# Performance work log

Hardware: AMD Instinct MI355X
Metric: run time of the kernel (lower is better)

## Reference

```python
import jax, jax.numpy as jnp
import numpy as np
from jax import lax

K = 3          # kernel_size
G = 8          # group count in SIFA
EPS = 1e-5     # BN and GN eps


def _bn(x, g, b, m, v):
    # eval-mode BatchNorm2d over channel dim 1
    scale = (g / jnp.sqrt(v + EPS))[None, :, None, None]
    shift = (b - m * g / jnp.sqrt(v + EPS))[None, :, None, None]
    return x * scale + shift


def setup_inputs() -> dict:
    key = jax.random.key(0)
    ks = jax.random.split(key, 20)
    B, C, H, W, OUP = 8, 64, 128, 128, 128
    CE = C * K * K  # expanded channels = 576
    CG = C // G     # channels per group view = 8
    f32 = jnp.float32
    inp = {
        "x": jax.random.normal(ks[0], (B, C, H, W), f32),
        # depthwise generate conv: groups=C, out=C*K^2 -> OIHW [CE,1,K,K]
        "gen_w": jax.random.normal(ks[1], (CE, 1, K, K), f32) * 0.1,
        "gen_bn_g": jnp.ones((CE,), f32) + 0.1 * jax.random.normal(ks[2], (CE,), f32),
        "gen_bn_b": 0.1 * jax.random.normal(ks[3], (CE,), f32),
        "gen_bn_m": 0.05 * jax.random.normal(ks[4], (CE,), f32),
        "gen_bn_v": jax.random.uniform(ks[5], (CE,), f32, 0.5, 1.5),
        # GroupNorm(num_groups=CG, num_channels=CG) affine params
        "gn_w": jnp.ones((CG,), f32) + 0.1 * jax.random.normal(ks[6], (CG,), f32),
        "gn_b": 0.1 * jax.random.normal(ks[7], (CG,), f32),
        # gating params, shape (1, CG, 1, 1)
        "cweight": 0.1 * jax.random.normal(ks[8], (1, CG, 1, 1), f32),
        "cbias": jnp.ones((1, CG, 1, 1), f32) + 0.1 * jax.random.normal(ks[9], (1, CG, 1, 1), f32),
        "sweight": 0.1 * jax.random.normal(ks[10], (1, CG, 1, 1), f32),
        "sbias": jnp.ones((1, CG, 1, 1), f32) + 0.1 * jax.random.normal(ks[11], (1, CG, 1, 1), f32),
        "weights_add": jnp.asarray(0.5, f32),
        # final Conv: C -> OUP, k=K, s=K, p=0, bias=False + BN + SiLU
        "conv_w": jax.random.normal(ks[12], (OUP, C, K, K), f32) * (1.0 / np.sqrt(C * K * K)),
        "conv_bn_g": jnp.ones((OUP,), f32) + 0.1 * jax.random.normal(ks[13], (OUP,), f32),
        "conv_bn_b": 0.1 * jax.random.normal(ks[14], (OUP,), f32),
        "conv_bn_m": 0.05 * jax.random.normal(ks[15], (OUP,), f32),
        "conv_bn_v": jax.random.uniform(ks[16], (OUP,), f32, 0.5, 1.5),
    }
    return inp


def reference(x, gen_w, gen_bn_g, gen_bn_b, gen_bn_m, gen_bn_v,
              gn_w, gn_b, cweight, cbias, sweight, sbias, weights_add,
              conv_w, conv_bn_g, conv_bn_b, conv_bn_m, conv_bn_v):
    B, C, H, W = x.shape
    # --- generate: depthwise conv (groups=C) + BN + ReLU ---
    y = lax.conv_general_dilated(
        x, gen_w, window_strides=(1, 1), padding=[(K // 2, K // 2)] * 2,
        feature_group_count=C,
        dimension_numbers=("NCHW", "OIHW", "NCHW"))  # [B, C*K*K, H, W]
    y = jax.nn.relu(_bn(y, gen_bn_g, gen_bn_b, gen_bn_m, gen_bn_v))
    # --- rearrange 'b c (n1 n2) h w -> b c (h n1) (w n2)' ---
    y = y.reshape(B, C, K, K, H, W)          # (b, c, n1, n2, h, w)
    y = y.transpose(0, 1, 4, 2, 5, 3)        # (b, c, h, n1, w, n2)
    HK, WK = H * K, W * K
    y = y.reshape(B, C, HK, WK)
    # --- group view: (b*G, C//G, HK, WK) ---
    g = y.reshape(B * G, C // G, HK, WK)
    # channel gate: global avg pool -> affine -> sigmoid
    x_ch = jnp.mean(g, axis=(2, 3), keepdims=True)        # [B*G, CG, 1, 1]
    ch = g * jax.nn.sigmoid(cweight * x_ch + cbias)
    # spatial gate: per-channel GroupNorm (num_groups == num_channels)
    mu = jnp.mean(g, axis=(2, 3), keepdims=True)
    var = jnp.var(g, axis=(2, 3), keepdims=True)
    gnorm = (g - mu) / jnp.sqrt(var + EPS)
    gnorm = gnorm * gn_w[None, :, None, None] + gn_b[None, :, None, None]
    sp = g * jax.nn.sigmoid(sweight * gnorm + sbias)
    out = weights_add * ch + (1.0 - weights_add) * sp
    out = out.reshape(B, C, HK, WK)
    # --- final Conv: k=K, s=K, p=0, no bias + BN + SiLU ---
    z = lax.conv_general_dilated(
        out, conv_w, window_strides=(K, K), padding="VALID",
        dimension_numbers=("NCHW", "OIHW", "NCHW"))       # [B, OUP, H, W]
    z = _bn(z, conv_bn_g, conv_bn_b, conv_bn_m, conv_bn_v)
    return z * jax.nn.sigmoid(z)  # SiLU
```

## Files before the change

kernel.cpp:

```cpp
#include <hip/hip_runtime.h>
#include <math.h>


#define EPSF 1e-5f
typedef _Float16 v8h __attribute__((ext_vector_type(8)));
typedef __fp16 fp16x2 __attribute__((ext_vector_type(2)));
typedef float v4f __attribute__((ext_vector_type(4)));

static constexpr int C_ = 64, HW_ = 16384, W_ = 128;
static constexpr int KB_ = 80;

static constexpr int WS_WFOLD = 0;
static constexpr int WS_SHIFT = 5184;
static constexpr int WS_BIAS  = 5760;
static constexpr int WS_GATE  = 5888;
static constexpr int WS_PART  = 7936;
static constexpr int WS_WH    = 73472;
static constexpr int WS_BIMG  = 114688;
static constexpr size_t BIMG_BATCH_F16 = (size_t)128 * KB_ * 128 * 8;
static constexpr size_t BIMG_BATCH_FLT = BIMG_BATCH_F16 / 2;

__device__ __forceinline__ float sigmf(float v) { return 1.f / (1.f + __expf(-v)); }

__device__ __forceinline__ unsigned int pk_u32(float a, float b) {
    fp16x2 h = __builtin_amdgcn_cvt_pkrtz(a, b);
    return __builtin_bit_cast(unsigned int, h);
}

__global__ __launch_bounds__(256) void k_fold(
    const float* __restrict__ gen_w,
    const float* __restrict__ gg, const float* __restrict__ gb,
    const float* __restrict__ gm, const float* __restrict__ gv,
    const float* __restrict__ conv_w,
    const float* __restrict__ cg, const float* __restrict__ cb,
    const float* __restrict__ cm, const float* __restrict__ cv,
    float* __restrict__ ws)
{
    int idx = blockIdx.x * 256 + threadIdx.x;
    _Float16* Whp = (_Float16*)(ws + WS_WH);
    if (idx < 81920) {
        int kb = idx >> 10, oup = (idx >> 3) & 127, e = idx & 7;
        int k = kb * 8 + e;
        int grp = k / 80, rr = k - grp * 80;
        int tp = rr / 40, vv = rr - tp * 40;
        float v = 0.f;
        if (vv < 36) {
            int j = vv >> 2, cl = vv & 3, c = grp * 8 + tp * 4 + cl;
            float s = cg[oup] * rsqrtf(cv[oup] + EPSF);
            v = conv_w[(oup * C_ + c) * 9 + j] * s;
        }
        Whp[idx] = (_Float16)v;
    } else if (idx < 87104) {
        int i = idx - 81920; int ce = i / 9;
        float s = gg[ce] * rsqrtf(gv[ce] + EPSF);
        ws[WS_WFOLD + i] = gen_w[i] * s;
    } else if (idx < 87680) {
        int ce = idx - 87104;
        float s = gg[ce] * rsqrtf(gv[ce] + EPSF);
        ws[WS_SHIFT + ce] = gb[ce] - gm[ce] * s;
    } else if (idx < 87808) {
        int oup = idx - 87680;
        float s = cg[oup] * rsqrtf(cv[oup] + EPSF);
        ws[WS_BIAS + oup] = cb[oup] - cm[oup] * s;
    }
}

__global__ __launch_bounds__(256) void k_conv(
    const float* __restrict__ x, float* __restrict__ ws, int b0)
{
    __shared__ float xs[4][18 * 19];
    __shared__ unsigned int ul[256 * 22];
    __shared__ float red[4][8];
    int bid = blockIdx.x;
    int cq = bid & 15, p = (bid >> 4) & 63, bbl = bid >> 10;
    int b = b0 + bbl;
    int oh0 = (p >> 3) << 4, ow0 = (p & 7) << 4;
    int t = threadIdx.x;
    int row16 = t >> 4, col = t & 15;

    for (int i = t; i < 1296; i += 256) {
        int ch = i / 324, rr = i - ch * 324;
        int r = rr / 18, cc = rr - r * 18;
        int yy = oh0 + r - 1, xx = ow0 + cc - 1;
        float v = 0.f;
        if (yy >= 0 && yy < 128 && xx >= 0 && xx < 128)
            v = x[(size_t)(b * C_ + cq * 4 + ch) * HW_ + yy * 128 + xx];
        xs[ch][r * 19 + cc] = v;
    }
    __syncthreads();

    float nb4[4][9];
#pragma unroll
    for (int ch = 0; ch < 4; ++ch)
#pragma unroll
        for (int dy = 0; dy < 3; ++dy)
#pragma unroll
            for (int dx = 0; dx < 3; ++dx)
                nb4[ch][dy * 3 + dx] = xs[ch][(row16 + dy) * 19 + col + dx];

    float st[8];
#pragma unroll
    for (int k = 0; k < 8; ++k) st[k] = 0.f;

#pragma unroll 1
    for (int j = 0; j < 9; ++j) {
        float wj[4][9], sj[4];
#pragma unroll
        for (int ch = 0; ch < 4; ++ch) {
            const float* wp = ws + WS_WFOLD + (cq * 4 + ch) * 81 + j * 9;
#pragma unroll
            for (int k = 0; k < 9; ++k) wj[ch][k] = wp[k];
            sj[ch] = ws[WS_SHIFT + (cq * 4 + ch) * 9 + j];
        }
        float uv[4];
#pragma unroll
        for (int ch = 0; ch < 4; ++ch) {
            float a = sj[ch];
#pragma unroll
            for (int k = 0; k < 9; ++k) a = fmaf(wj[ch][k], nb4[ch][k], a);
            float v = fmaxf(a, 0.f);
            uv[ch] = v;
            st[ch * 2] += v;
            st[ch * 2 + 1] = fmaf(v, v, st[ch * 2 + 1]);
        }
        uint2 pk;
        pk.x = pk_u32(uv[0], uv[1]);
        pk.y = pk_u32(uv[2], uv[3]);
        int ci = j >> 1;
        *(uint2*)&ul[t * 22 + ci * 4 + (j & 1) * 2] = pk;
    }
    {
        uint2 z; z.x = 0u; z.y = 0u;
        *(uint2*)&ul[t * 22 + 18] = z;
    }

    int tile = ((p >> 3) * 2 + (row16 >> 3)) * 8 + (p & 7);
    int px = (row16 & 7) * 16 + col;
    int kbBase = (cq >> 1) * 10 + (cq & 1) * 5;
    _Float16* Bimg = (_Float16*)(ws + WS_BIMG) + (size_t)bbl * BIMG_BATCH_F16;
#pragma unroll
    for (int ci = 0; ci < 5; ++ci) {
        uint2 lo = *(uint2*)&ul[t * 22 + ci * 4];
        uint2 hi = *(uint2*)&ul[t * 22 + ci * 4 + 2];
        uint4 cell; cell.x = lo.x; cell.y = lo.y; cell.z = hi.x; cell.w = hi.y;
        *(uint4*)(Bimg + (size_t)(tile * KB_ + kbBase + ci) * 1024 + (size_t)px * 8) = cell;
    }

#pragma unroll
    for (int off = 32; off > 0; off >>= 1)
#pragma unroll
        for (int k = 0; k < 8; ++k) st[k] += __shfl_down(st[k], off, 64);
    int w = t >> 6, lane = t & 63;
    if (lane == 0)
#pragma unroll
        for (int k = 0; k < 8; ++k) red[w][k] = st[k];
    __syncthreads();
    if (t < 8) {
        float v = red[0][t] + red[1][t] + red[2][t] + red[3][t];
        float* part = ws + WS_PART;
        part[(size_t)((b * 16 + cq) * 8 + t) * 64 + p] = v;
    }
}

__global__ __launch_bounds__(256) void k_gate(
    const float* __restrict__ part,
    const float* __restrict__ cwt, const float* __restrict__ cbs,
    const float* __restrict__ swt, const float* __restrict__ sbs,
    const float* __restrict__ gnw, const float* __restrict__ gnb,
    const float* __restrict__ wadd, float4* __restrict__ gate, int b0, int nb)
{
    int i = blockIdx.x * 256 + threadIdx.x;
    if (i >= nb * 64) return;
    int b = b0 + (i >> 6), c = i & 63;
    const float* pp = part + (size_t)((b * 16 + (c >> 2)) * 8 + (c & 3) * 2) * 64;
    float s1 = 0.f, s2 = 0.f;
#pragma unroll
    for (int q = 0; q < 16; ++q) {
        float4 a = *(const float4*)(pp + q * 4);
        float4 d = *(const float4*)(pp + 64 + q * 4);
        s1 += a.x + a.y + a.z + a.w;
        s2 += d.x + d.y + d.z + d.w;
    }
    const float N = 9.f * 16384.f;
    float mean = s1 / N;
    float var = s2 / N - mean * mean;
    float inv = rsqrtf(var + EPSF);
    int cgi = c & 7;
    float wa = wadd[0];
    float cgt = sigmf(cwt[cgi] * mean + cbs[cgi]);
    const float NL2E = -1.44269504f;
    float4 o;
    o.x = wa * cgt;
    o.y = 1.f - wa;
    o.z = NL2E * (swt[cgi] * gnw[cgi] * inv);
    o.w = NL2E * (swt[cgi] * (gnb[cgi] - mean * inv * gnw[cgi]) + sbs[cgi]);
    gate[b * 64 + c] = o;
}

__global__ __launch_bounds__(256, 4) void k_main(
    const float* __restrict__ ws, float* __restrict__ out, int b0)
{
    __shared__ _Float16 Bs[40 * 512];
    int t = threadIdx.x;
    int bid = blockIdx.x;
    int half = bid & 1, tile = (bid >> 1) & 127, bbl = bid >> 8;
    int b = b0 + bbl;
    int oh0 = (tile >> 3) << 3, ow0 = (tile & 7) << 4;

    int w = __builtin_amdgcn_readfirstlane(t >> 6);
    int lane = t & 63, quad = lane >> 4, l15 = lane & 15;

    const _Float16* Wh = (const _Float16*)(ws + WS_WH);
    const _Float16* Bimg = (const _Float16*)(ws + WS_BIMG)
        + (size_t)bbl * BIMG_BATCH_F16 + (size_t)tile * (KB_ * 1024)
        + (size_t)(half * 64 + lane) * 8;
    const float4* gp = (const float4*)(ws + WS_GATE) + b * 64;

    v4f acc[2][4];
#pragma unroll
    for (int a = 0; a < 2; ++a)
#pragma unroll
        for (int bb = 0; bb < 4; ++bb) acc[a][bb] = (v4f)0.f;

#pragma unroll 1
    for (int r = 0; r < 2; ++r) {
        if (r) __syncthreads();
#pragma unroll 2
        for (int i = 0; i < 10; ++i) {
            int kl = i * 4 + w;
            int kb = r * 40 + kl;
            int q5 = kb / 10;
            int cbase = q5 * 8 + (kb - q5 * 10 >= 5 ? 4 : 0);
            float4 g0 = gp[cbase], g1 = gp[cbase + 1];
            float4 g2 = gp[cbase + 2], g3 = gp[cbase + 3];
            uint4 cell = *(const uint4*)(Bimg + (size_t)kb * 1024);
            v8h v = __builtin_bit_cast(v8h, cell);
            float u[8];
#pragma unroll
            for (int e = 0; e < 8; ++e) {
                float f = (float)v[e];
                float4 g = (e & 3) == 0 ? g0 : ((e & 3) == 1 ? g1 : ((e & 3) == 2 ? g2 : g3));
                float ex = __builtin_amdgcn_exp2f(fmaf(g.z, f, g.w));
                u[e] = f * fmaf(g.y, __builtin_amdgcn_rcpf(1.f + ex), g.x);
            }
            uint4 oc;
            oc.x = pk_u32(u[0], u[1]); oc.y = pk_u32(u[2], u[3]);
            oc.z = pk_u32(u[4], u[5]); oc.w = pk_u32(u[6], u[7]);
            *(uint4*)(Bs + kl * 512 + lane * 8) = oc;
        }
        __syncthreads();
#pragma unroll
        for (int s = 0; s < 10; ++s) {
            int cglob = r * 40 + s * 4 + quad;
            const _Float16* Ap = Wh + ((size_t)cglob * 128 + w * 32 + l15) * 8;
            v8h A0 = *(const v8h*)(Ap);
            v8h A1 = *(const v8h*)(Ap + 128);
            int klq = s * 4 + quad;
            v8h Bf[4];
#pragma unroll
            for (int bb = 0; bb < 4; ++bb)
                Bf[bb] = *(const v8h*)(Bs + klq * 512 + (bb * 16 + l15) * 8);
#pragma unroll
            for (int bb = 0; bb < 4; ++bb) {
                acc[0][bb] = __builtin_amdgcn_mfma_f32_16x16x32_f16(A0, Bf[bb], acc[0][bb], 0, 0, 0);
                acc[1][bb] = __builtin_amdgcn_mfma_f32_16x16x32_f16(A1, Bf[bb], acc[1][bb], 0, 0, 0);
            }
        }
    }

    size_t ob = (size_t)b * 128 * HW_;
#pragma unroll
    for (int a = 0; a < 2; ++a) {
#pragma unroll
        for (int r2 = 0; r2 < 4; ++r2) {
            int oup = w * 32 + a * 16 + quad * 4 + r2;
            float bo = ws[WS_BIAS + oup];
#pragma unroll
            for (int bb = 0; bb < 4; ++bb) {
                int p2 = half * 64 + bb * 16 + l15;
                int py2 = p2 >> 4, px2 = p2 & 15;
                float z = acc[a][bb][r2] + bo;
                out[ob + (size_t)oup * HW_ + (oh0 + py2) * W_ + ow0 + px2] = z * sigmf(z);
            }
        }
    }
}

extern "C" void kernel_launch(void* const* d_in, const int* in_sizes, int n_in,
                              void* d_out, int out_size, void* d_ws, size_t ws_size,
                              hipStream_t stream)
{
    const float* x      = (const float*)d_in[0];
    const float* gen_w  = (const float*)d_in[1];
    const float* gg     = (const float*)d_in[2];
    const float* gb     = (const float*)d_in[3];
    const float* gm     = (const float*)d_in[4];
    const float* gv     = (const float*)d_in[5];
    const float* gnw    = (const float*)d_in[6];
    const float* gnb    = (const float*)d_in[7];
    const float* cwt    = (const float*)d_in[8];
    const float* cbs    = (const float*)d_in[9];
    const float* swt    = (const float*)d_in[10];
    const float* sbs    = (const float*)d_in[11];
    const float* wadd   = (const float*)d_in[12];
    const float* conv_w = (const float*)d_in[13];
    const float* cg2    = (const float*)d_in[14];
    const float* cb2    = (const float*)d_in[15];
    const float* cm2    = (const float*)d_in[16];
    const float* cv2    = (const float*)d_in[17];
    float* ws  = (float*)d_ws;
    float* out = (float*)d_out;

    size_t avail = ws_size / 4;
    int nb = 1;
    const int cands[4] = {8, 4, 2, 1};
    for (int i = 0; i < 4; ++i) {
        if ((size_t)WS_BIMG + (size_t)cands[i] * BIMG_BATCH_FLT <= avail) { nb = cands[i]; break; }
    }

    k_fold<<<343, 256, 0, stream>>>(gen_w, gg, gb, gm, gv, conv_w, cg2, cb2, cm2, cv2, ws);
    for (int b0 = 0; b0 < 8; b0 += nb) {
        k_conv<<<nb * 1024, 256, 0, stream>>>(x, ws, b0);
        k_gate<<<(nb * 64 + 255) / 256, 256, 0, stream>>>(
            ws + WS_PART, cwt, cbs, swt, sbs, gnw, gnb, wadd,
            (float4*)(ws + WS_GATE), b0, nb);
        k_main<<<nb * 256, 256, 0, stream>>>(ws, out, b0);
    }
}
```

Baseline: 236.7 us.

## Reorder K layout to per-channel 8-tap cells and give each wave one channel

Changes the packing of the expanded-channel K dimension. Each 8-wide cell now holds taps 0-7 of one channel, and a fifth cell per group holds tap 8 for four channels, replacing the previous interleaving of 4 channels by 2 taps. The depthwise conv kernel now assigns one channel per wave with its 81 weights in registers, writes cells directly without the large LDS staging buffer, and reduces stats per wave, which lowers LDS use and shuffle work. The gate kernel loads a single gate vector for most cells and handles only four values in the tap-8 cell. Register pressure in the conv kernel rises because of the 81 weights held per thread.

```diff
diff --git a/kernel.cpp b/kernel.cpp
--- a/kernel.cpp
+++ b/kernel.cpp
@@ -40,12 +40,14 @@
     _Float16* Whp = (_Float16*)(ws + WS_WH);
     if (idx < 81920) {
         int kb = idx >> 10, oup = (idx >> 3) & 127, e = idx & 7;
-        int k = kb * 8 + e;
-        int grp = k / 80, rr = k - grp * 80;
-        int tp = rr / 40, vv = rr - tp * 40;
+        int grp = kb / 10, r = kb - grp * 10;
+        int tp = r / 5, cl = r - tp * 5;
+        int cbase = grp * 8 + tp * 4;
+        int c = -1, j = 0;
+        if (cl < 4) { c = cbase + cl; j = e; }
+        else if (e < 4) { c = cbase + e; j = 8; }
         float v = 0.f;
-        if (vv < 36) {
-            int j = vv >> 2, cl = vv & 3, c = grp * 8 + tp * 4 + cl;
+        if (c >= 0) {
             float s = cg[oup] * rsqrtf(cv[oup] + EPSF);
             v = conv_w[(oup * C_ + c) * 9 + j] * s;
         }
@@ -69,14 +71,13 @@
     const float* __restrict__ x, float* __restrict__ ws, int b0)
 {
     __shared__ float xs[4][18 * 19];
-    __shared__ unsigned int ul[256 * 22];
-    __shared__ float red[4][8];
+    __shared__ float wfl[4][96];
+    __shared__ unsigned short j8l[4][256];
     int bid = blockIdx.x;
     int cq = bid & 15, p = (bid >> 4) & 63, bbl = bid >> 10;
     int b = b0 + bbl;
     int oh0 = (p >> 3) << 4, ow0 = (p & 7) << 4;
     int t = threadIdx.x;
-    int row16 = t >> 4, col = t & 15;
 
     for (int i = t; i < 1296; i += 256) {
         int ch = i / 324, rr = i - ch * 324;
@@ -87,78 +88,90 @@
             v = x[(size_t)(b * C_ + cq * 4 + ch) * HW_ + yy * 128 + xx];
         xs[ch][r * 19 + cc] = v;
     }
+    for (int i = t; i < 384; i += 256) {
+        int ch = i / 96, k = i - ch * 96;
+        int c = cq * 4 + ch;
+        float v = 0.f;
+        if (k < 81) v = ws[WS_WFOLD + c * 81 + k];
+        else if (k >= 84 && k < 93) v = ws[WS_SHIFT + c * 9 + (k - 84)];
+        wfl[ch][k] = v;
+    }
     __syncthreads();
 
-    float nb4[4][9];
-#pragma unroll
-    for (int ch = 0; ch < 4; ++ch)
+    int w = __builtin_amdgcn_readfirstlane(t >> 6);
+    int lane = t & 63, r0 = lane >> 4, col = lane & 15;
+
+    float wv[81], sh9[9];
+#pragma unroll
+    for (int i = 0; i < 20; ++i) {
+        float4 v4 = *(const float4*)&wfl[w][i * 4];
+        wv[i * 4] = v4.x; wv[i * 4 + 1] = v4.y; wv[i * 4 + 2] = v4.z; wv[i * 4 + 3] = v4.w;
+    }
+    wv[80] = wfl[w][80];
+#pragma unroll
+    for (int i = 0; i < 9; ++i) sh9[i] = wfl[w][84 + i];
+
+    float st0 = 0.f, st1 = 0.f;
+    int kbBase = (cq >> 1) * 10 + (cq & 1) * 5;
+    int tileBase = ((p >> 3) * 2) * 8 + (p & 7);
+    _Float16* Bimg = (_Float16*)(ws + WS_BIMG) + (size_t)bbl * BIMG_BATCH_F16;
+
+#pragma unroll 1
+    for (int i = 0; i < 4; ++i) {
+        int row16 = r0 + 4 * i;
+        float nb[9];
 #pragma unroll
         for (int dy = 0; dy < 3; ++dy)
 #pragma unroll
             for (int dx = 0; dx < 3; ++dx)
-                nb4[ch][dy * 3 + dx] = xs[ch][(row16 + dy) * 19 + col + dx];
-
-    float st[8];
-#pragma unroll
-    for (int k = 0; k < 8; ++k) st[k] = 0.f;
-
-#pragma unroll 1
-    for (int j = 0; j < 9; ++j) {
-        float wj[4][9], sj[4];
-#pragma unroll
-        for (int ch = 0; ch < 4; ++ch) {
-            const float* wp = ws + WS_WFOLD + (cq * 4 + ch) * 81 + j * 9;
-#pragma unroll
-            for (int k = 0; k < 9; ++k) wj[ch][k] = wp[k];
-            sj[ch] = ws[WS_SHIFT + (cq * 4 + ch) * 9 + j];
-        }
-        float uv[4];
-#pragma unroll
-        for (int ch = 0; ch < 4; ++ch) {
-            float a = sj[ch];
-#pragma unroll
-            for (int k = 0; k < 9; ++k) a = fmaf(wj[ch][k], nb4[ch][k], a);
-            float v = fmaxf(a, 0.f);
-            uv[ch] = v;
-            st[ch * 2] += v;
-            st[ch * 2 + 1] = fmaf(v, v, st[ch * 2 + 1]);
-        }
-        uint2 pk;
-        pk.x = pk_u32(uv[0], uv[1]);
-        pk.y = pk_u32(uv[2], uv[3]);
-        int ci = j >> 1;
-        *(uint2*)&ul[t * 22 + ci * 4 + (j & 1) * 2] = pk;
-    }
+                nb[dy * 3 + dx] = xs[w][(row16 + dy) * 19 + col + dx];
+        float uv[9];
+#pragma unroll
+        for (int j = 0; j < 9; ++j) uv[j] = sh9[j];
+#pragma unroll
+        for (int k = 0; k < 9; ++k) {
+            float xv = nb[k];
+#pragma unroll
+            for (int j = 0; j < 9; ++j) uv[j] = fmaf(wv[j * 9 + k], xv, uv[j]);
+        }
+#pragma unroll
+        for (int j = 0; j < 9; ++j) {
+            float v = fmaxf(uv[j], 0.f);
+            uv[j] = v;
+            st0 += v;
+            st1 = fmaf(v, v, st1);
+        }
+        int tile = tileBase + (row16 >> 3) * 8;
+        int px = (row16 & 7) * 16 + col;
+        uint4 oc;
+        oc.x = pk_u32(uv[0], uv[1]); oc.y = pk_u32(uv[2], uv[3]);
+        oc.z = pk_u32(uv[4], uv[5]); oc.w = pk_u32(uv[6], uv[7]);
+        *(uint4*)(Bimg + (size_t)(tile * KB_ + kbBase + w) * 1024 + (size_t)px * 8) = oc;
+        _Float16 h8 = (_Float16)uv[8];
+        j8l[w][row16 * 16 + col] = __builtin_bit_cast(unsigned short, h8);
+    }
+    __syncthreads();
+
     {
-        uint2 z; z.x = 0u; z.y = 0u;
-        *(uint2*)&ul[t * 22 + 18] = z;
-    }
-
-    int tile = ((p >> 3) * 2 + (row16 >> 3)) * 8 + (p & 7);
-    int px = (row16 & 7) * 16 + col;
-    int kbBase = (cq >> 1) * 10 + (cq & 1) * 5;
-    _Float16* Bimg = (_Float16*)(ws + WS_BIMG) + (size_t)bbl * BIMG_BATCH_F16;
-#pragma unroll
-    for (int ci = 0; ci < 5; ++ci) {
-        uint2 lo = *(uint2*)&ul[t * 22 + ci * 4];
-        uint2 hi = *(uint2*)&ul[t * 22 + ci * 4 + 2];
-        uint4 cell; cell.x = lo.x; cell.y = lo.y; cell.z = hi.x; cell.w = hi.y;
-        *(uint4*)(Bimg + (size_t)(tile * KB_ + kbBase + ci) * 1024 + (size_t)px * 8) = cell;
-    }
-
-#pragma unroll
-    for (int off = 32; off > 0; off >>= 1)
-#pragma unroll
-        for (int k = 0; k < 8; ++k) st[k] += __shfl_down(st[k], off, 64);
-    int w = t >> 6, lane = t & 63;
-    if (lane == 0)
-#pragma unroll
-        for (int k = 0; k < 8; ++k) red[w][k] = st[k];
-    __syncthreads();
-    if (t < 8) {
-        float v = red[0][t] + red[1][t] + red[2][t] + red[3][t];
+        int row16 = t >> 4;
+        int tile = tileBase + (row16 >> 3) * 8;
+        int px = t & 127;
+        uint4 oc;
+        oc.x = (unsigned int)j8l[0][t] | ((unsigned int)j8l[1][t] << 16);
+        oc.y = (unsigned int)j8l[2][t] | ((unsigned int)j8l[3][t] << 16);
+        oc.z = 0u; oc.w = 0u;
+        *(uint4*)(Bimg + (size_t)(tile * KB_ + kbBase + 4) * 1024 + (size_t)px * 8) = oc;
+    }
+
+#pragma unroll
+    for (int off = 32; off > 0; off >>= 1) {
+        st0 += __shfl_down(st0, off, 64);
+        st1 += __shfl_down(st1, off, 64);
+    }
+    if (lane == 0) {
         float* part = ws + WS_PART;
-        part[(size_t)((b * 16 + cq) * 8 + t) * 64 + p] = v;
+        part[(size_t)((b * 16 + cq) * 8 + w * 2) * 64 + p] = st0;
+        part[(size_t)((b * 16 + cq) * 8 + w * 2 + 1) * 64 + p] = st1;
     }
 }
 
@@ -229,23 +242,37 @@
         for (int i = 0; i < 10; ++i) {
             int kl = i * 4 + w;
             int kb = r * 40 + kl;
-            int q5 = kb / 10;
-            int cbase = q5 * 8 + (kb - q5 * 10 >= 5 ? 4 : 0);
-            float4 g0 = gp[cbase], g1 = gp[cbase + 1];
-            float4 g2 = gp[cbase + 2], g3 = gp[cbase + 3];
+            int grp = kb / 10, rr = kb - grp * 10;
+            int tp = (rr >= 5) ? 1 : 0, cl = rr - tp * 5;
+            int cbase = grp * 8 + tp * 4;
             uint4 cell = *(const uint4*)(Bimg + (size_t)kb * 1024);
             v8h v = __builtin_bit_cast(v8h, cell);
-            float u[8];
-#pragma unroll
-            for (int e = 0; e < 8; ++e) {
-                float f = (float)v[e];
-                float4 g = (e & 3) == 0 ? g0 : ((e & 3) == 1 ? g1 : ((e & 3) == 2 ? g2 : g3));
-                float ex = __builtin_amdgcn_exp2f(fmaf(g.z, f, g.w));
-                u[e] = f * fmaf(g.y, __builtin_amdgcn_rcpf(1.f + ex), g.x);
+            uint4 oc;
+            if (cl < 4) {
+                float4 g = gp[cbase + cl];
+                float u[8];
+#pragma unroll
+                for (int e = 0; e < 8; ++e) {
+                    float f = (float)v[e];
+                    float ex = __builtin_amdgcn_exp2f(fmaf(g.z, f, g.w));
+                    u[e] = f * fmaf(g.y, __builtin_amdgcn_rcpf(1.f + ex), g.x);
+                }
+                oc.x = pk_u32(u[0], u[1]); oc.y = pk_u32(u[2], u[3]);
+                oc.z = pk_u32(u[4], u[5]); oc.w = pk_u32(u[6], u[7]);
+            } else {
+                float4 g0 = gp[cbase], g1 = gp[cbase + 1];
+                float4 g2 = gp[cbase + 2], g3 = gp[cbase + 3];
+                float u[4];
+#pragma unroll
+                for (int e = 0; e < 4; ++e) {
+                    float f = (float)v[e];
+                    float4 g = (e == 0) ? g0 : ((e == 1) ? g1 : ((e == 2) ? g2 : g3));
+                    float ex = __builtin_amdgcn_exp2f(fmaf(g.z, f, g.w));
+                    u[e] = f * fmaf(g.y, __builtin_amdgcn_rcpf(1.f + ex), g.x);
+                }
+                oc.x = pk_u32(u[0], u[1]); oc.y = pk_u32(u[2], u[3]);
+                oc.z = 0u; oc.w = 0u;
             }
-            uint4 oc;
-            oc.x = pk_u32(u[0], u[1]); oc.y = pk_u32(u[2], u[3]);
-            oc.z = pk_u32(u[4], u[5]); oc.w = pk_u32(u[6], u[7]);
             *(uint4*)(Bs + kl * 512 + lane * 8) = oc;
         }
         __syncthreads();
```

Result: no change. 241.3 us (+1.9%).
